# Performance work log

Measured on AMD Instinct MI355X. Metric: run time of the kernel, lower is better.

## Reference

```python
import jax, jax.numpy as jnp
import numpy as np

N_NODES = 50000
N_EDGES = 800000
IN, HID, OUT = 128, [128, 128], 64


def setup_inputs() -> dict:
    key = jax.random.key(0)
    ks = jax.random.split(key, 10)
    inp = {
        'in_feat': jax.random.normal(ks[0], (N_NODES, IN), dtype=jnp.float32),
        'src': jax.random.randint(ks[1], (N_EDGES,), 0, N_NODES, dtype=jnp.int32),
        'dst': jax.random.randint(ks[2], (N_EDGES,), 0, N_NODES, dtype=jnp.int32),
    }
    dims = [IN] + HID + [OUT]  # [128,128,128,64]
    for i in range(3):
        fan_in = dims[i]
        inp[f'W{i}'] = jax.random.normal(ks[3 + i], (dims[i + 1], dims[i]), dtype=jnp.float32) / np.sqrt(fan_in)
        inp[f'b{i}'] = jnp.zeros((dims[i + 1],), dtype=jnp.float32)
    return inp


def _sage_gcn_layer(x, W, b, src, dst, n_nodes):
    # DGL SAGEConv aggregator_type='gcn':
    #   neigh = segment_sum of src feats over dst edges (graph already has self-loops)
    #   h = (neigh + x) / (in_degree + 1); out = h @ W.T + b
    msg = x[src]                                             # [E, d] gather
    neigh = jax.ops.segment_sum(msg, dst, num_segments=n_nodes)
    deg = jax.ops.segment_sum(jnp.ones(src.shape[0], x.dtype), dst, num_segments=n_nodes)
    h = (neigh + x) / (deg[:, None] + 1.0)
    return h @ W.T + b


def reference(in_feat, src, dst, W0, b0, W1, b1, W2, b2):
    n = in_feat.shape[0]
    # remove_self_loop + add_self_loop -> exactly one self loop per node
    loop = jnp.arange(n, dtype=src.dtype)
    src_f = jnp.concatenate([src, loop])
    dst_f = jnp.concatenate([dst, loop])
    # Dropout(0.5) is identity in eval mode.
    h = in_feat
    h = jax.nn.relu(_sage_gcn_layer(h, W0, b0, src_f, dst_f, n))
    h = jax.nn.relu(_sage_gcn_layer(h, W1, b1, src_f, dst_f, n))
    h = _sage_gcn_layer(h, W2, b2, src_f, dst_f, n)
    return h
```

## Files before the change

kernel.cpp:

```cpp
#include <hip/hip_runtime.h>
#include <hip/hip_bf16.h>


#define NFEAT 128
#define BKT_CAP 12288
#define CHUNK 64

using bf16x8 = __attribute__((ext_vector_type(8))) short;
using f32x4  = __attribute__((ext_vector_type(4))) float;

__device__ __forceinline__ ushort f2bf(float f) {
    unsigned u = __float_as_uint(f);
    u = (u + 0x7fffu + ((u >> 16) & 1u)) >> 16;
    return (ushort)u;
}
__device__ __forceinline__ float bflo(unsigned v) { return __uint_as_float(v << 16); }
__device__ __forceinline__ float bfhi(unsigned v) { return __uint_as_float(v & 0xffff0000u); }

__device__ __forceinline__ int xcc_id() {
    int x;
    asm volatile("s_getreg_b32 %0, hwreg(HW_REG_XCC_ID)" : "=s"(x));
    return x & 7;
}


__global__ __launch_bounds__(1024) void k_zero_words(int* __restrict__ p, int n) {
    int i = threadIdx.x;
    if (i < n) p[i] = 0;
}

__global__ __launch_bounds__(256) void k_bin(const int* __restrict__ src, const int* __restrict__ dst,
                                             int* __restrict__ gcur, unsigned* __restrict__ pairs, int ne) {
    __shared__ int lcnt[128];
    __shared__ int lbase[128];
    int tid = threadIdx.x;
    if (tid < 128) lcnt[tid] = 0;
    __syncthreads();
    int e0 = blockIdx.x * 4096;
    int myrank[16];
    int mybkt[16];
    unsigned mypair[16];
    #pragma unroll
    for (int i = 0; i < 16; ++i) {
        int e = e0 + tid + i * 256;
        if (e < ne) {
            int s = src[e], d = dst[e];
            int b = d >> 9;
            mybkt[i]  = b;
            mypair[i] = (unsigned)(s & 0xffff) | ((unsigned)(d & 511) << 16);
            myrank[i] = atomicAdd(&lcnt[b], 1);
        } else mybkt[i] = -1;
    }
    __syncthreads();
    if (tid < 128) lbase[tid] = lcnt[tid] ? atomicAdd(&gcur[tid], lcnt[tid]) : 0;
    __syncthreads();
    #pragma unroll
    for (int i = 0; i < 16; ++i) {
        if (mybkt[i] >= 0) {
            int pos = lbase[mybkt[i]] + myrank[i];
            if (pos < BKT_CAP) pairs[(size_t)mybkt[i] * BKT_CAP + pos] = mypair[i];
        }
    }
}

__global__ __launch_bounds__(256) void k_cnt(const unsigned* __restrict__ pairs, const int* __restrict__ gcur,
                                             int* __restrict__ cnt, int n) {
    __shared__ int lcnt[512];
    int b = blockIdx.x, tid = threadIdx.x;
    for (int i = tid; i < 512; i += 256) lcnt[i] = 0;
    __syncthreads();
    int m = gcur[b];
    if (m > BKT_CAP) m = BKT_CAP;
    const unsigned* p = pairs + (size_t)b * BKT_CAP;
    for (int i = tid; i < m; i += 256) atomicAdd(&lcnt[p[i] >> 16], 1);
    __syncthreads();
    int base = b * 512;
    for (int i = tid; i < 512; i += 256) {
        int node = base + i;
        if (node < n) cnt[node] = lcnt[i];
    }
}

__global__ __launch_bounds__(1024) void k_scan_part(const int* __restrict__ cnt, int* __restrict__ part,
                                                    int* __restrict__ tots, int n) {
    __shared__ int wtot[16];
    __shared__ int wpre[16];
    int tid  = threadIdx.x;
    int lane = tid & 63;
    int wv   = tid >> 6;
    int i    = blockIdx.x * 1024 + tid;
    int v    = (i < n) ? cnt[i] : 0;
    int val  = v;
    #pragma unroll
    for (int off = 1; off < 64; off <<= 1) {
        int t = __shfl_up(val, off);
        if (lane >= off) val += t;
    }
    if (lane == 63) wtot[wv] = val;
    __syncthreads();
    if (tid == 0) {
        int s = 0;
        #pragma unroll
        for (int w = 0; w < 16; ++w) { wpre[w] = s; s += wtot[w]; }
        tots[blockIdx.x] = s;
    }
    __syncthreads();
    int excl = val - v + wpre[wv];
    if (i < n) part[i] = excl;
}

__global__ __launch_bounds__(1024) void k_scan_tops(int* __restrict__ tots, int* __restrict__ total_out, int nch) {
    __shared__ int wtot[16];
    __shared__ int wpre[16];
    int tid  = threadIdx.x;
    int lane = tid & 63;
    int wv   = tid >> 6;
    int v    = (tid < nch) ? tots[tid] : 0;
    int val  = v;
    #pragma unroll
    for (int off = 1; off < 64; off <<= 1) {
        int t = __shfl_up(val, off);
        if (lane >= off) val += t;
    }
    if (lane == 63) wtot[wv] = val;
    __syncthreads();
    if (tid == 0) {
        int s = 0;
        #pragma unroll
        for (int w = 0; w < 16; ++w) { wpre[w] = s; s += wtot[w]; }
        *total_out = s;
    }
    __syncthreads();
    int excl = val - v + wpre[wv];
    if (tid < nch) tots[tid] = excl;
}

__global__ __launch_bounds__(1024) void k_scan_add(int* __restrict__ offs, const int* __restrict__ tots, int n) {
    int i = blockIdx.x * 1024 + threadIdx.x;
    if (i < n) offs[i] += tots[blockIdx.x];
}

__global__ __launch_bounds__(256) void k_scatter(const unsigned* __restrict__ pairs, const int* __restrict__ gcur,
                                                 const int* __restrict__ offs, ushort* __restrict__ esrc, int n) {
    __shared__ int lcur[512];
    __shared__ int loffs[512];
    int b = blockIdx.x, tid = threadIdx.x;
    int base = b * 512;
    for (int i = tid; i < 512; i += 256) {
        lcur[i] = 0;
        int node = base + i;
        loffs[i] = (node < n) ? offs[node] : 0;
    }
    __syncthreads();
    int m = gcur[b];
    if (m > BKT_CAP) m = BKT_CAP;
    const unsigned* p = pairs + (size_t)b * BKT_CAP;
    for (int i = tid; i < m; i += 256) {
        unsigned pr = p[i];
        int dlow = pr >> 16;
        int r = atomicAdd(&lcur[dlow], 1);
        esrc[loffs[dlow] + r] = (ushort)(pr & 0xffffu);
    }
}


__global__ __launch_bounds__(1024) void k_dsort_win(const int* __restrict__ cnt, int* __restrict__ perm, int n) {
    __shared__ int hist[256];
    __shared__ int hcur[256];
    __shared__ int wtot[16];
    __shared__ int wpre[16];
    int tid  = threadIdx.x;
    int base = blockIdx.x * 1024;
    if (tid < 256) hist[tid] = 0;
    __syncthreads();
    int i = base + tid;
    bool act = i < n;
    int d = 0, rank = 0;
    if (act) {
        d = cnt[i];
        if (d > 255) d = 255;
        rank = atomicAdd(&hist[d], 1);
    }
    __syncthreads();
    int lane = tid & 63;
    int wv   = tid >> 6;
    int v    = (tid < 256) ? hist[tid] : 0;
    int val  = v;
    #pragma unroll
    for (int off = 1; off < 64; off <<= 1) {
        int t = __shfl_up(val, off);
        if (lane >= off) val += t;
    }
    if (lane == 63) wtot[wv] = val;
    __syncthreads();
    if (tid == 0) {
        int s = 0;
        #pragma unroll
        for (int w = 0; w < 4; ++w) { wpre[w] = s; s += wtot[w]; }
    }
    __syncthreads();
    if (tid < 256) hcur[tid] = val - v + wpre[wv];
    __syncthreads();
    if (act) perm[base + hcur[d] + rank] = i;
}


__global__ __launch_bounds__(256) void k_cast3(const float* __restrict__ a, int na,
                                               const float* __restrict__ b, int nb,
                                               const float* __restrict__ c, int nc,
                                               ushort* __restrict__ out) {
    int i = blockIdx.x * 256 + threadIdx.x;
    if (i >= na + nb + nc) return;
    float v = (i < na) ? a[i] : ((i < na + nb) ? b[i - na] : c[i - na - nb]);
    out[i] = f2bf(v);
}


template <typename InT, int N, bool PLANES_IN>
__global__ __launch_bounds__(256) void k_gemm_mfma(const InT* __restrict__ X, const ushort* __restrict__ Wb,
                                                   ushort* __restrict__ Y, int M) {
    int w    = threadIdx.x >> 6;
    int lane = threadIdx.x & 63;
    int rowf = blockIdx.x * 64 + w * 16 + (lane & 15);
    int kb   = (lane >> 4) * 8;

    bf16x8 a[4];
    if (rowf < M) {
        #pragma unroll
        for (int ks = 0; ks < 4; ++ks) {
            if constexpr (PLANES_IN) {
                a[ks] = *(const bf16x8*)((const ushort*)X + (size_t)ks * M * 32 + (size_t)rowf * 32 + kb);
            } else {
                const float* xp = (const float*)X + (size_t)rowf * 128 + ks * 32 + kb;
                float4 f0 = *(const float4*)xp;
                float4 f1 = *(const float4*)(xp + 4);
                bf16x8 t;
                t[0] = f2bf(f0.x); t[1] = f2bf(f0.y); t[2] = f2bf(f0.z); t[3] = f2bf(f0.w);
                t[4] = f2bf(f1.x); t[5] = f2bf(f1.y); t[6] = f2bf(f1.z); t[7] = f2bf(f1.w);
                a[ks] = t;
            }
        }
    } else {
        #pragma unroll
        for (int ks = 0; ks < 4; ++ks) {
            bf16x8 z = {0, 0, 0, 0, 0, 0, 0, 0};
            a[ks] = z;
        }
    }

    constexpr int NT = N / 16;
    f32x4 acc[NT];
    #pragma unroll
    for (int nt = 0; nt < NT; ++nt) acc[nt] = (f32x4){0.f, 0.f, 0.f, 0.f};

    #pragma unroll
    for (int nt = 0; nt < NT; ++nt) {
        const ushort* wp = Wb + (size_t)(nt * 16 + (lane & 15)) * 128 + kb;
        #pragma unroll
        for (int ks = 0; ks < 4; ++ks) {
            bf16x8 b = *(const bf16x8*)(wp + ks * 32);
            acc[nt] = __builtin_amdgcn_mfma_f32_16x16x32_bf16(a[ks], b, acc[nt], 0, 0, 0);
        }
    }

    int c  = lane & 15;
    int r0 = blockIdx.x * 64 + w * 16 + (lane >> 4) * 4;
    #pragma unroll
    for (int j = 0; j < 4; ++j) {
        int r = r0 + j;
        if (r < M) {
            #pragma unroll
            for (int nt = 0; nt < NT; ++nt)
                Y[(size_t)(nt >> 1) * M * 32 + (size_t)r * 32 + (nt & 1) * 16 + c] = (ushort)f2bf(acc[nt][j]);
        }
    }
}


#define ACC8(T)  { a0 += bflo((T).x); a1 += bfhi((T).x); a2 += bflo((T).y); a3 += bfhi((T).y); \
                   a4 += bflo((T).z); a5 += bfhi((T).z); a6 += bflo((T).w); a7 += bfhi((T).w); }

template <bool RELU>
__global__ __launch_bounds__(256) void k_agg128(const ushort* __restrict__ Yp, const int* __restrict__ offs,
                                                const ushort* __restrict__ esrc, const float* __restrict__ bias,
                                                ushort* __restrict__ Zp, const int* __restrict__ perm,
                                                int* __restrict__ qh, int n, int nchunk) {
    __shared__ int sQ, sT;
    if (threadIdx.x == 0) {
        int pref = xcc_id() & 3;
        int t = -1, qsel = 0;
        #pragma unroll
        for (int a = 0; a < 4; ++a) {
            int cand = (pref + a) & 3;
            int tt = atomicAdd(&qh[cand * 16], 1);
            if (tt < nchunk) { qsel = cand; t = tt; break; }
        }
        sQ = qsel; sT = t;
    }
    __syncthreads();
    int q = sQ, t = sT;
    if (t < 0) return;
    int lane = threadIdx.x & 63;
    int wv   = threadIdx.x >> 6;
    int g    = lane >> 2;
    int sub  = lane & 3;
    int idx  = t * CHUNK + wv * 16 + g;
    bool active = idx < n;
    int nd = 0, start = 0, rem = 0;
    if (active) {
        nd    = perm[idx];
        start = offs[nd];
        rem   = offs[nd + 1] - start;
    }
    const uint4* Y4 = (const uint4*)(Yp + (size_t)q * n * 32);
    uint4*       Z4 = (uint4*)(Zp + (size_t)q * n * 32);

    float a0 = 0.f, a1 = 0.f, a2 = 0.f, a3 = 0.f, a4 = 0.f, a5 = 0.f, a6 = 0.f, a7 = 0.f;

    int minrem = rem, maxrem = rem;
    #pragma unroll
    for (int m = 4; m < 64; m <<= 1) {
        minrem = min(minrem, __shfl_xor(minrem, m));
        maxrem = max(maxrem, __shfl_xor(maxrem, m));
    }

    int r = 0;
    for (; r + 8 <= minrem; r += 8) {
        int e = start + r;
        int s0 = esrc[e],     s1 = esrc[e + 1], s2 = esrc[e + 2], s3 = esrc[e + 3];
        int s4 = esrc[e + 4], s5 = esrc[e + 5], s6 = esrc[e + 6], s7 = esrc[e + 7];
        uint4 t0 = Y4[(size_t)s0 * 4 + sub];
        uint4 t1 = Y4[(size_t)s1 * 4 + sub];
        uint4 t2 = Y4[(size_t)s2 * 4 + sub];
        uint4 t3 = Y4[(size_t)s3 * 4 + sub];
        uint4 t4 = Y4[(size_t)s4 * 4 + sub];
        uint4 t5 = Y4[(size_t)s5 * 4 + sub];
        uint4 t6 = Y4[(size_t)s6 * 4 + sub];
        uint4 t7 = Y4[(size_t)s7 * 4 + sub];
        ACC8(t0); ACC8(t1); ACC8(t2); ACC8(t3); ACC8(t4); ACC8(t5); ACC8(t6); ACC8(t7);
    }
    for (; r + 4 <= minrem; r += 4) {
        int e = start + r;
        int s0 = esrc[e], s1 = esrc[e + 1], s2 = esrc[e + 2], s3 = esrc[e + 3];
        uint4 t0 = Y4[(size_t)s0 * 4 + sub];
        uint4 t1 = Y4[(size_t)s1 * 4 + sub];
        uint4 t2 = Y4[(size_t)s2 * 4 + sub];
        uint4 t3 = Y4[(size_t)s3 * 4 + sub];
        ACC8(t0); ACC8(t1); ACC8(t2); ACC8(t3);
    }
    for (; r < maxrem; r += 4) {
        #pragma unroll
        for (int c = 0; c < 4; ++c) {
            int rr = r + c;
            bool val = rr < rem;
            int e = val ? (start + rr) : 0;
            int s = esrc[e];
            uint4 tv = Y4[(size_t)s * 4 + sub];
            if (!val) { tv.x = 0u; tv.y = 0u; tv.z = 0u; tv.w = 0u; }
            ACC8(tv);
        }
    }

    if (active) {
        float scale = 1.0f / (float)(rem + 2);
        uint4 sf = Y4[(size_t)nd * 4 + sub];
        int f0 = q * 32 + sub * 8;
        float4 bA = *(const float4*)&bias[f0];
        float4 bB = *(const float4*)&bias[f0 + 4];
        float r0 = (a0 + 2.f * bflo(sf.x)) * scale + bA.x;
        float r1 = (a1 + 2.f * bfhi(sf.x)) * scale + bA.y;
        float r2 = (a2 + 2.f * bflo(sf.y)) * scale + bA.z;
        float r3 = (a3 + 2.f * bfhi(sf.y)) * scale + bA.w;
        float r4 = (a4 + 2.f * bflo(sf.z)) * scale + bB.x;
        float r5 = (a5 + 2.f * bfhi(sf.z)) * scale + bB.y;
        float r6 = (a6 + 2.f * bflo(sf.w)) * scale + bB.z;
        float r7 = (a7 + 2.f * bfhi(sf.w)) * scale + bB.w;
        if (RELU) {
            r0 = fmaxf(r0, 0.f); r1 = fmaxf(r1, 0.f); r2 = fmaxf(r2, 0.f); r3 = fmaxf(r3, 0.f);
            r4 = fmaxf(r4, 0.f); r5 = fmaxf(r5, 0.f); r6 = fmaxf(r6, 0.f); r7 = fmaxf(r7, 0.f);
        }
        uint4 o;
        o.x = (unsigned)f2bf(r0) | ((unsigned)f2bf(r1) << 16);
        o.y = (unsigned)f2bf(r2) | ((unsigned)f2bf(r3) << 16);
        o.z = (unsigned)f2bf(r4) | ((unsigned)f2bf(r5) << 16);
        o.w = (unsigned)f2bf(r6) | ((unsigned)f2bf(r7) << 16);
        Z4[(size_t)nd * 4 + sub] = o;
    }
}

__global__ __launch_bounds__(256) void k_agg64(const ushort* __restrict__ Yp, const int* __restrict__ offs,
                                               const ushort* __restrict__ esrc, const float* __restrict__ bias,
                                               float* __restrict__ Z, const int* __restrict__ perm,
                                               int* __restrict__ qh, int n, int nchunk) {
    __shared__ int sQ, sT;
    if (threadIdx.x == 0) {
        int pref = xcc_id() & 1;
        int t = -1, qsel = 0;
        #pragma unroll
        for (int a = 0; a < 2; ++a) {
            int cand = (pref + a) & 1;
            int tt = atomicAdd(&qh[cand * 16], 1);
            if (tt < nchunk) { qsel = cand; t = tt; break; }
        }
        sQ = qsel; sT = t;
    }
    __syncthreads();
    int h = sQ, t = sT;
    if (t < 0) return;
    int lane = threadIdx.x & 63;
    int wv   = threadIdx.x >> 6;
    int g    = lane >> 2;
    int sub  = lane & 3;
    int idx  = t * CHUNK + wv * 16 + g;
    bool active = idx < n;
    int nd = 0, start = 0, rem = 0;
    if (active) {
        nd    = perm[idx];
        start = offs[nd];
        rem   = offs[nd + 1] - start;
    }
    const uint4* Y4 = (const uint4*)(Yp + (size_t)h * n * 32);

    float a0 = 0.f, a1 = 0.f, a2 = 0.f, a3 = 0.f, a4 = 0.f, a5 = 0.f, a6 = 0.f, a7 = 0.f;

    int minrem = rem, maxrem = rem;
    #pragma unroll
    for (int m = 4; m < 64; m <<= 1) {
        minrem = min(minrem, __shfl_xor(minrem, m));
        maxrem = max(maxrem, __shfl_xor(maxrem, m));
    }

    int r = 0;
    for (; r + 8 <= minrem; r += 8) {
        int e = start + r;
        int s0 = esrc[e],     s1 = esrc[e + 1], s2 = esrc[e + 2], s3 = esrc[e + 3];
        int s4 = esrc[e + 4], s5 = esrc[e + 5], s6 = esrc[e + 6], s7 = esrc[e + 7];
        uint4 t0 = Y4[(size_t)s0 * 4 + sub];
        uint4 t1 = Y4[(size_t)s1 * 4 + sub];
        uint4 t2 = Y4[(size_t)s2 * 4 + sub];
        uint4 t3 = Y4[(size_t)s3 * 4 + sub];
        uint4 t4 = Y4[(size_t)s4 * 4 + sub];
        uint4 t5 = Y4[(size_t)s5 * 4 + sub];
        uint4 t6 = Y4[(size_t)s6 * 4 + sub];
        uint4 t7 = Y4[(size_t)s7 * 4 + sub];
        ACC8(t0); ACC8(t1); ACC8(t2); ACC8(t3); ACC8(t4); ACC8(t5); ACC8(t6); ACC8(t7);
    }
    for (; r + 4 <= minrem; r += 4) {
        int e = start + r;
        int s0 = esrc[e], s1 = esrc[e + 1], s2 = esrc[e + 2], s3 = esrc[e + 3];
        uint4 t0 = Y4[(size_t)s0 * 4 + sub];
        uint4 t1 = Y4[(size_t)s1 * 4 + sub];
        uint4 t2 = Y4[(size_t)s2 * 4 + sub];
        uint4 t3 = Y4[(size_t)s3 * 4 + sub];
        ACC8(t0); ACC8(t1); ACC8(t2); ACC8(t3);
    }
    for (; r < maxrem; r += 4) {
        #pragma unroll
        for (int c = 0; c < 4; ++c) {
            int rr = r + c;
            bool val = rr < rem;
            int e = val ? (start + rr) : 0;
            int s = esrc[e];
            uint4 tv = Y4[(size_t)s * 4 + sub];
            if (!val) { tv.x = 0u; tv.y = 0u; tv.z = 0u; tv.w = 0u; }
            ACC8(tv);
        }
    }

    if (active) {
        float scale = 1.0f / (float)(rem + 2);
        uint4 sf = Y4[(size_t)nd * 4 + sub];
        int f0 = h * 32 + sub * 8;
        float4 bA = *(const float4*)&bias[f0];
        float4 bB = *(const float4*)&bias[f0 + 4];
        float4 oA, oB;
        oA.x = (a0 + 2.f * bflo(sf.x)) * scale + bA.x;
        oA.y = (a1 + 2.f * bfhi(sf.x)) * scale + bA.y;
        oA.z = (a2 + 2.f * bflo(sf.y)) * scale + bA.z;
        oA.w = (a3 + 2.f * bfhi(sf.y)) * scale + bA.w;
        oB.x = (a4 + 2.f * bflo(sf.z)) * scale + bB.x;
        oB.y = (a5 + 2.f * bfhi(sf.z)) * scale + bB.y;
        oB.z = (a6 + 2.f * bflo(sf.w)) * scale + bB.z;
        oB.w = (a7 + 2.f * bfhi(sf.w)) * scale + bB.w;
        float* zr = Z + (size_t)nd * 64 + f0;
        *(float4*)zr       = oA;
        *(float4*)(zr + 4) = oB;
    }
}


extern "C" void kernel_launch(void* const* d_in, const int* in_sizes, int n_in,
                              void* d_out, int out_size, void* d_ws, size_t ws_size,
                              hipStream_t stream) {
    const float* in_feat = (const float*)d_in[0];
    const int*   src     = (const int*)d_in[1];
    const int*   dst     = (const int*)d_in[2];
    const float* W0      = (const float*)d_in[3];
    const float* b0      = (const float*)d_in[4];
    const float* W1      = (const float*)d_in[5];
    const float* b1      = (const float*)d_in[6];
    const float* W2      = (const float*)d_in[7];
    const float* b2      = (const float*)d_in[8];
    float* out = (float*)d_out;

    const int n  = in_sizes[0] / NFEAT;
    const int ne = in_sizes[1];
    const int nch = (n + 1023) / 1024;
    const int NB  = (n + 511) >> 9;
    const int nchunk = (n + CHUNK - 1) / CHUNK;

    int* offs       = (int*)d_ws;
    int* tots       = offs + (((n + 1) + 3) & ~3);
    int* gcur       = tots + 1024;
    int* qh         = gcur + 128;
    int* cnt        = qh + 192;
    int* perm       = cnt + ((n + 3) & ~3);
    unsigned* pairs = (unsigned*)(perm + ((n + 3) & ~3));
    ushort* esrc    = (ushort*)(pairs + (size_t)128 * BKT_CAP);
    ushort* Wb      = esrc + ((ne + 15) & ~15);
    ushort* Ybuf    = Wb + 40960;
    ushort* Zbuf    = Ybuf + (size_t)n * NFEAT;

    k_zero_words<<<1, 1024, 0, stream>>>(gcur, 128 + 192);
    k_bin<<<(ne + 4095) / 4096, 256, 0, stream>>>(src, dst, gcur, pairs, ne);
    k_cnt<<<NB, 256, 0, stream>>>(pairs, gcur, cnt, n);
    k_dsort_win<<<nch, 1024, 0, stream>>>(cnt, perm, n);
    k_scan_part<<<nch, 1024, 0, stream>>>(cnt, offs, tots, n);
    k_scan_tops<<<1, 1024, 0, stream>>>(tots, offs + n, nch);
    k_scan_add<<<nch, 1024, 0, stream>>>(offs, tots, n);
    k_scatter<<<NB, 256, 0, stream>>>(pairs, gcur, offs, esrc, n);

    k_cast3<<<(40960 + 255) / 256, 256, 0, stream>>>(W0, 16384, W1, 16384, W2, 8192, Wb);
    const ushort* Wb0 = Wb;
    const ushort* Wb1 = Wb + 16384;
    const ushort* Wb2 = Wb + 32768;

    const int gg = (n + 63) / 64;

    k_gemm_mfma<float, 128, false><<<gg, 256, 0, stream>>>(in_feat, Wb0, Ybuf, n);
    k_agg128<true><<<4 * nchunk, 256, 0, stream>>>(Ybuf, offs, esrc, b0, Zbuf, perm, qh, n, nchunk);
    k_gemm_mfma<ushort, 128, true><<<gg, 256, 0, stream>>>(Zbuf, Wb1, Ybuf, n);
    k_agg128<true><<<4 * nchunk, 256, 0, stream>>>(Ybuf, offs, esrc, b1, Zbuf, perm, qh + 64, n, nchunk);
    k_gemm_mfma<ushort, 64, true><<<gg, 256, 0, stream>>>(Zbuf, Wb2, Ybuf, n);
    k_agg64<<<2 * nchunk, 256, 0, stream>>>(Ybuf, offs, esrc, b2, out, perm, qh + 128, n, nchunk);

    (void)ws_size; (void)n_in; (void)out_size;
}
```

Baseline: 222.1 us.

## Pad CSR rows to multiples of eight with sentinel zero row for branchless gathers

```diff
diff --git a/kernel.cpp b/kernel.cpp
--- a/kernel.cpp
+++ b/kernel.cpp
@@ -24,10 +24,20 @@
 }
 
 
-__global__ __launch_bounds__(1024) void k_zero_words(int* __restrict__ p, int n) {
-    int i = threadIdx.x;
-    if (i < n) p[i] = 0;
-}
+__global__ __launch_bounds__(256) void k_init(unsigned* __restrict__ esrc_u32, int fillN, unsigned sent2,
+                                              int* __restrict__ ctl, ushort* __restrict__ Ybuf, int n) {
+    int i = blockIdx.x * 256 + threadIdx.x;
+    if (i < fillN) {
+        esrc_u32[i] = sent2;
+    } else if (i < fillN + 320) {
+        ctl[i - fillN] = 0;
+    } else if (i < fillN + 320 + 64) {
+        int j = i - fillN - 320;
+        int p = j >> 4, k = j & 15;
+        ((unsigned*)(Ybuf + (size_t)p * (n + 1) * 32 + (size_t)n * 32))[k] = 0u;
+    }
+}
+
 
 __global__ __launch_bounds__(256) void k_bin(const int* __restrict__ src, const int* __restrict__ dst,
                                              int* __restrict__ gcur, unsigned* __restrict__ pairs, int ne) {
@@ -81,32 +91,67 @@
     }
 }
 
-__global__ __launch_bounds__(1024) void k_scan_part(const int* __restrict__ cnt, int* __restrict__ part,
-                                                    int* __restrict__ tots, int n) {
+__global__ __launch_bounds__(1024) void k_prep_win(const int* __restrict__ cnt, int* __restrict__ perm,
+                                                   int* __restrict__ part, int* __restrict__ tots, int n) {
+    __shared__ int hist[256];
+    __shared__ int hcur[256];
     __shared__ int wtot[16];
     __shared__ int wpre[16];
     int tid  = threadIdx.x;
     int lane = tid & 63;
     int wv   = tid >> 6;
-    int i    = blockIdx.x * 1024 + tid;
-    int v    = (i < n) ? cnt[i] : 0;
-    int val  = v;
-    #pragma unroll
-    for (int off = 1; off < 64; off <<= 1) {
-        int t = __shfl_up(val, off);
-        if (lane >= off) val += t;
-    }
-    if (lane == 63) wtot[wv] = val;
-    __syncthreads();
-    if (tid == 0) {
-        int s = 0;
-        #pragma unroll
-        for (int w = 0; w < 16; ++w) { wpre[w] = s; s += wtot[w]; }
-        tots[blockIdx.x] = s;
-    }
-    __syncthreads();
-    int excl = val - v + wpre[wv];
-    if (i < n) part[i] = excl;
+    int base = blockIdx.x * 1024;
+    if (tid < 256) hist[tid] = 0;
+    __syncthreads();
+    int i = base + tid;
+    bool act = i < n;
+    int c = 0, d = 0, rank = 0;
+    if (act) {
+        c = cnt[i];
+        d = c > 255 ? 255 : c;
+        rank = atomicAdd(&hist[d], 1);
+    }
+    __syncthreads();
+    {
+        int v = (tid < 256) ? hist[tid] : 0;
+        int val = v;
+        #pragma unroll
+        for (int off = 1; off < 64; off <<= 1) {
+            int t = __shfl_up(val, off);
+            if (lane >= off) val += t;
+        }
+        if (lane == 63) wtot[wv] = val;
+        __syncthreads();
+        if (tid == 0) {
+            int s = 0;
+            #pragma unroll
+            for (int w = 0; w < 4; ++w) { wpre[w] = s; s += wtot[w]; }
+        }
+        __syncthreads();
+        if (tid < 256) hcur[tid] = val - v + wpre[wv];
+        __syncthreads();
+        if (act) perm[base + hcur[d] + rank] = i;
+        __syncthreads();
+    }
+    {
+        int p = act ? ((c + 7) & ~7) : 0;
+        int val = p;
+        #pragma unroll
+        for (int off = 1; off < 64; off <<= 1) {
+            int t = __shfl_up(val, off);
+            if (lane >= off) val += t;
+        }
+        if (lane == 63) wtot[wv] = val;
+        __syncthreads();
+        if (tid == 0) {
+            int s = 0;
+            #pragma unroll
+            for (int w = 0; w < 16; ++w) { wpre[w] = s; s += wtot[w]; }
+            tots[blockIdx.x] = s;
+        }
+        __syncthreads();
+        if (act) part[i] = val - p + wpre[wv];
+    }
 }
 
 __global__ __launch_bounds__(1024) void k_scan_tops(int* __restrict__ tots, int* __restrict__ total_out, int nch) {
@@ -164,47 +209,6 @@
 }
 
 
-__global__ __launch_bounds__(1024) void k_dsort_win(const int* __restrict__ cnt, int* __restrict__ perm, int n) {
-    __shared__ int hist[256];
-    __shared__ int hcur[256];
-    __shared__ int wtot[16];
-    __shared__ int wpre[16];
-    int tid  = threadIdx.x;
-    int base = blockIdx.x * 1024;
-    if (tid < 256) hist[tid] = 0;
-    __syncthreads();
-    int i = base + tid;
-    bool act = i < n;
-    int d = 0, rank = 0;
-    if (act) {
-        d = cnt[i];
-        if (d > 255) d = 255;
-        rank = atomicAdd(&hist[d], 1);
-    }
-    __syncthreads();
-    int lane = tid & 63;
-    int wv   = tid >> 6;
-    int v    = (tid < 256) ? hist[tid] : 0;
-    int val  = v;
-    #pragma unroll
-    for (int off = 1; off < 64; off <<= 1) {
-        int t = __shfl_up(val, off);
-        if (lane >= off) val += t;
-    }
-    if (lane == 63) wtot[wv] = val;
-    __syncthreads();
-    if (tid == 0) {
-        int s = 0;
-        #pragma unroll
-        for (int w = 0; w < 4; ++w) { wpre[w] = s; s += wtot[w]; }
-    }
-    __syncthreads();
-    if (tid < 256) hcur[tid] = val - v + wpre[wv];
-    __syncthreads();
-    if (act) perm[base + hcur[d] + rank] = i;
-}
-
-
 __global__ __launch_bounds__(256) void k_cast3(const float* __restrict__ a, int na,
                                                const float* __restrict__ b, int nb,
                                                const float* __restrict__ c, int nc,
@@ -218,7 +222,7 @@
 
 template <typename InT, int N, bool PLANES_IN>
 __global__ __launch_bounds__(256) void k_gemm_mfma(const InT* __restrict__ X, const ushort* __restrict__ Wb,
-                                                   ushort* __restrict__ Y, int M) {
+                                                   ushort* __restrict__ Y, int M, int Mp) {
     int w    = threadIdx.x >> 6;
     int lane = threadIdx.x & 63;
     int rowf = blockIdx.x * 64 + w * 16 + (lane & 15);
@@ -229,7 +233,7 @@
         #pragma unroll
         for (int ks = 0; ks < 4; ++ks) {
             if constexpr (PLANES_IN) {
-                a[ks] = *(const bf16x8*)((const ushort*)X + (size_t)ks * M * 32 + (size_t)rowf * 32 + kb);
+                a[ks] = *(const bf16x8*)((const ushort*)X + (size_t)ks * Mp * 32 + (size_t)rowf * 32 + kb);
             } else {
                 const float* xp = (const float*)X + (size_t)rowf * 128 + ks * 32 + kb;
                 float4 f0 = *(const float4*)xp;
@@ -271,7 +275,7 @@
         if (r < M) {
             #pragma unroll
             for (int nt = 0; nt < NT; ++nt)
-                Y[(size_t)(nt >> 1) * M * 32 + (size_t)r * 32 + (nt & 1) * 16 + c] = (ushort)f2bf(acc[nt][j]);
+                Y[(size_t)(nt >> 1) * Mp * 32 + (size_t)r * 32 + (nt & 1) * 16 + c] = (ushort)f2bf(acc[nt][j]);
         }
     }
 }
@@ -282,9 +286,10 @@
 
 template <bool RELU>
 __global__ __launch_bounds__(256) void k_agg128(const ushort* __restrict__ Yp, const int* __restrict__ offs,
-                                                const ushort* __restrict__ esrc, const float* __restrict__ bias,
-                                                ushort* __restrict__ Zp, const int* __restrict__ perm,
-                                                int* __restrict__ qh, int n, int nchunk) {
+                                                const int* __restrict__ cnt, const ushort* __restrict__ esrc,
+                                                const float* __restrict__ bias, ushort* __restrict__ Zp,
+                                                const int* __restrict__ perm, int* __restrict__ qh,
+                                                int n, int nchunk) {
     __shared__ int sQ, sT;
     if (threadIdx.x == 0) {
         int pref = xcc_id() & 3;
@@ -306,29 +311,27 @@
     int sub  = lane & 3;
     int idx  = t * CHUNK + wv * 16 + g;
     bool active = idx < n;
-    int nd = 0, start = 0, rem = 0;
+    int nd = 0, start = 0, deg = 0;
     if (active) {
         nd    = perm[idx];
         start = offs[nd];
-        rem   = offs[nd + 1] - start;
-    }
-    const uint4* Y4 = (const uint4*)(Yp + (size_t)q * n * 32);
-    uint4*       Z4 = (uint4*)(Zp + (size_t)q * n * 32);
+        deg   = cnt[nd];
+    }
+    const uint4* Y4 = (const uint4*)(Yp + (size_t)q * (n + 1) * 32);
+    uint4*       Z4 = (uint4*)(Zp + (size_t)q * (n + 1) * 32);
 
     float a0 = 0.f, a1 = 0.f, a2 = 0.f, a3 = 0.f, a4 = 0.f, a5 = 0.f, a6 = 0.f, a7 = 0.f;
 
-    int minrem = rem, maxrem = rem;
-    #pragma unroll
-    for (int m = 4; m < 64; m <<= 1) {
-        minrem = min(minrem, __shfl_xor(minrem, m));
-        maxrem = max(maxrem, __shfl_xor(maxrem, m));
-    }
-
-    int r = 0;
-    for (; r + 8 <= minrem; r += 8) {
-        int e = start + r;
-        int s0 = esrc[e],     s1 = esrc[e + 1], s2 = esrc[e + 2], s3 = esrc[e + 3];
-        int s4 = esrc[e + 4], s5 = esrc[e + 5], s6 = esrc[e + 6], s7 = esrc[e + 7];
+    int nblk = active ? ((deg + 7) >> 3) : 0;
+    const uint4* ep = (const uint4*)(esrc + start);
+    uint4 ib = ep[0];
+    #pragma unroll 2
+    for (int b = 0; b < nblk; ++b) {
+        uint4 ibn = ep[b + 1];
+        unsigned s0 = ib.x & 0xffffu, s1 = ib.x >> 16;
+        unsigned s2 = ib.y & 0xffffu, s3 = ib.y >> 16;
+        unsigned s4 = ib.z & 0xffffu, s5 = ib.z >> 16;
+        unsigned s6 = ib.w & 0xffffu, s7 = ib.w >> 16;
         uint4 t0 = Y4[(size_t)s0 * 4 + sub];
         uint4 t1 = Y4[(size_t)s1 * 4 + sub];
         uint4 t2 = Y4[(size_t)s2 * 4 + sub];
@@ -338,31 +341,11 @@
         uint4 t6 = Y4[(size_t)s6 * 4 + sub];
         uint4 t7 = Y4[(size_t)s7 * 4 + sub];
         ACC8(t0); ACC8(t1); ACC8(t2); ACC8(t3); ACC8(t4); ACC8(t5); ACC8(t6); ACC8(t7);
-    }
-    for (; r + 4 <= minrem; r += 4) {
-        int e = start + r;
-        int s0 = esrc[e], s1 = esrc[e + 1], s2 = esrc[e + 2], s3 = esrc[e + 3];
-        uint4 t0 = Y4[(size_t)s0 * 4 + sub];
-        uint4 t1 = Y4[(size_t)s1 * 4 + sub];
-        uint4 t2 = Y4[(size_t)s2 * 4 + sub];
-        uint4 t3 = Y4[(size_t)s3 * 4 + sub];
-        ACC8(t0); ACC8(t1); ACC8(t2); ACC8(t3);
-    }
-    for (; r < maxrem; r += 4) {
-        #pragma unroll
-        for (int c = 0; c < 4; ++c) {
-            int rr = r + c;
-            bool val = rr < rem;
-            int e = val ? (start + rr) : 0;
-            int s = esrc[e];
-            uint4 tv = Y4[(size_t)s * 4 + sub];
-            if (!val) { tv.x = 0u; tv.y = 0u; tv.z = 0u; tv.w = 0u; }
-            ACC8(tv);
-        }
+        ib = ibn;
     }
 
     if (active) {
-        float scale = 1.0f / (float)(rem + 2);
+        float scale = 1.0f / (float)(deg + 2);
         uint4 sf = Y4[(size_t)nd * 4 + sub];
         int f0 = q * 32 + sub * 8;
         float4 bA = *(const float4*)&bias[f0];
@@ -389,9 +372,10 @@
 }
 
 __global__ __launch_bounds__(256) void k_agg64(const ushort* __restrict__ Yp, const int* __restrict__ offs,
-                                               const ushort* __restrict__ esrc, const float* __restrict__ bias,
-                                               float* __restrict__ Z, const int* __restrict__ perm,
-                                               int* __restrict__ qh, int n, int nchunk) {
+                                               const int* __restrict__ cnt, const ushort* __restrict__ esrc,
+                                               const float* __restrict__ bias, float* __restrict__ Z,
+                                               const int* __restrict__ perm, int* __restrict__ qh,
+                                               int n, int nchunk) {
     __shared__ int sQ, sT;
     if (threadIdx.x == 0) {
         int pref = xcc_id() & 1;
@@ -413,28 +397,26 @@
     int sub  = lane & 3;
     int idx  = t * CHUNK + wv * 16 + g;
     bool active = idx < n;
-    int nd = 0, start = 0, rem = 0;
+    int nd = 0, start = 0, deg = 0;
     if (active) {
         nd    = perm[idx];
         start = offs[nd];
-        rem   = offs[nd + 1] - start;
-    }
-    const uint4* Y4 = (const uint4*)(Yp + (size_t)h * n * 32);
+        deg   = cnt[nd];
+    }
+    const uint4* Y4 = (const uint4*)(Yp + (size_t)h * (n + 1) * 32);
 
     float a0 = 0.f, a1 = 0.f, a2 = 0.f, a3 = 0.f, a4 = 0.f, a5 = 0.f, a6 = 0.f, a7 = 0.f;
 
-    int minrem = rem, maxrem = rem;
-    #pragma unroll
-    for (int m = 4; m < 64; m <<= 1) {
-        minrem = min(minrem, __shfl_xor(minrem, m));
-        maxrem = max(maxrem, __shfl_xor(maxrem, m));
-    }
-
-    int r = 0;
-    for (; r + 8 <= minrem; r += 8) {
-        int e = start + r;
-        int s0 = esrc[e],     s1 = esrc[e + 1], s2 = esrc[e + 2], s3 = esrc[e + 3];
-        int s4 = esrc[e + 4], s5 = esrc[e + 5], s6 = esrc[e + 6], s7 = esrc[e + 7];
+    int nblk = active ? ((deg + 7) >> 3) : 0;
+    const uint4* ep = (const uint4*)(esrc + start);
+    uint4 ib = ep[0];
+    #pragma unroll 2
+    for (int b = 0; b < nblk; ++b) {
+        uint4 ibn = ep[b + 1];
+        unsigned s0 = ib.x & 0xffffu, s1 = ib.x >> 16;
+        unsigned s2 = ib.y & 0xffffu, s3 = ib.y >> 16;
+        unsigned s4 = ib.z & 0xffffu, s5 = ib.z >> 16;
+        unsigned s6 = ib.w & 0xffffu, s7 = ib.w >> 16;
         uint4 t0 = Y4[(size_t)s0 * 4 + sub];
         uint4 t1 = Y4[(size_t)s1 * 4 + sub];
         uint4 t2 = Y4[(size_t)s2 * 4 + sub];
@@ -444,31 +426,11 @@
         uint4 t6 = Y4[(size_t)s6 * 4 + sub];
         uint4 t7 = Y4[(size_t)s7 * 4 + sub];
         ACC8(t0); ACC8(t1); ACC8(t2); ACC8(t3); ACC8(t4); ACC8(t5); ACC8(t6); ACC8(t7);
-    }
-    for (; r + 4 <= minrem; r += 4) {
-        int e = start + r;
-        int s0 = esrc[e], s1 = esrc[e + 1], s2 = esrc[e + 2], s3 = esrc[e + 3];
-        uint4 t0 = Y4[(size_t)s0 * 4 + sub];
-        uint4 t1 = Y4[(size_t)s1 * 4 + sub];
-        uint4 t2 = Y4[(size_t)s2 * 4 + sub];
-        uint4 t3 = Y4[(size_t)s3 * 4 + sub];
-        ACC8(t0); ACC8(t1); ACC8(t2); ACC8(t3);
-    }
-    for (; r < maxrem; r += 4) {
-        #pragma unroll
-        for (int c = 0; c < 4; ++c) {
-            int rr = r + c;
-            bool val = rr < rem;
-            int e = val ? (start + rr) : 0;
-            int s = esrc[e];
-            uint4 tv = Y4[(size_t)s * 4 + sub];
-            if (!val) { tv.x = 0u; tv.y = 0u; tv.z = 0u; tv.w = 0u; }
-            ACC8(tv);
-        }
+        ib = ibn;
     }
 
     if (active) {
-        float scale = 1.0f / (float)(rem + 2);
+        float scale = 1.0f / (float)(deg + 2);
         uint4 sf = Y4[(size_t)nd * 4 + sub];
         int f0 = h * 32 + sub * 8;
         float4 bA = *(const float4*)&bias[f0];
@@ -508,6 +470,7 @@
     const int nch = (n + 1023) / 1024;
     const int NB  = (n + 511) >> 9;
     const int nchunk = (n + CHUNK - 1) / CHUNK;
+    const int escap = (ne + 8 * n + 31) & ~15;
 
     int* offs       = (int*)d_ws;
     int* tots       = offs + (((n + 1) + 3) & ~3);
@@ -517,15 +480,17 @@
     int* perm       = cnt + ((n + 3) & ~3);
     unsigned* pairs = (unsigned*)(perm + ((n + 3) & ~3));
     ushort* esrc    = (ushort*)(pairs + (size_t)128 * BKT_CAP);
-    ushort* Wb      = esrc + ((ne + 15) & ~15);
+    ushort* Wb      = esrc + escap;
     ushort* Ybuf    = Wb + 40960;
-    ushort* Zbuf    = Ybuf + (size_t)n * NFEAT;
-
-    k_zero_words<<<1, 1024, 0, stream>>>(gcur, 128 + 192);
+    ushort* Zbuf    = Ybuf + (size_t)(n + 1) * NFEAT;
+
+    const int fillN = escap / 2;
+    const unsigned sent2 = ((unsigned)n << 16) | (unsigned)n;
+    k_init<<<(fillN + 320 + 64 + 255) / 256, 256, 0, stream>>>((unsigned*)esrc, fillN, sent2, gcur, Ybuf, n);
+
     k_bin<<<(ne + 4095) / 4096, 256, 0, stream>>>(src, dst, gcur, pairs, ne);
     k_cnt<<<NB, 256, 0, stream>>>(pairs, gcur, cnt, n);
-    k_dsort_win<<<nch, 1024, 0, stream>>>(cnt, perm, n);
-    k_scan_part<<<nch, 1024, 0, stream>>>(cnt, offs, tots, n);
+    k_prep_win<<<nch, 1024, 0, stream>>>(cnt, perm, offs, tots, n);
     k_scan_tops<<<1, 1024, 0, stream>>>(tots, offs + n, nch);
     k_scan_add<<<nch, 1024, 0, stream>>>(offs, tots, n);
     k_scatter<<<NB, 256, 0, stream>>>(pairs, gcur, offs, esrc, n);
@@ -536,13 +501,14 @@
     const ushort* Wb2 = Wb + 32768;
 
     const int gg = (n + 63) / 64;
-
-    k_gemm_mfma<float, 128, false><<<gg, 256, 0, stream>>>(in_feat, Wb0, Ybuf, n);
-    k_agg128<true><<<4 * nchunk, 256, 0, stream>>>(Ybuf, offs, esrc, b0, Zbuf, perm, qh, n, nchunk);
-    k_gemm_mfma<ushort, 128, true><<<gg, 256, 0, stream>>>(Zbuf, Wb1, Ybuf, n);
-    k_agg128<true><<<4 * nchunk, 256, 0, stream>>>(Ybuf, offs, esrc, b1, Zbuf, perm, qh + 64, n, nchunk);
-    k_gemm_mfma<ushort, 64, true><<<gg, 256, 0, stream>>>(Zbuf, Wb2, Ybuf, n);
-    k_agg64<<<2 * nchunk, 256, 0, stream>>>(Ybuf, offs, esrc, b2, out, perm, qh + 128, n, nchunk);
+    const int Mp = n + 1;
+
+    k_gemm_mfma<float, 128, false><<<gg, 256, 0, stream>>>(in_feat, Wb0, Ybuf, n, Mp);
+    k_agg128<true><<<4 * nchunk, 256, 0, stream>>>(Ybuf, offs, cnt, esrc, b0, Zbuf, perm, qh, n, nchunk);
+    k_gemm_mfma<ushort, 128, true><<<gg, 256, 0, stream>>>(Zbuf, Wb1, Ybuf, n, Mp);
+    k_agg128<true><<<4 * nchunk, 256, 0, stream>>>(Ybuf, offs, cnt, esrc, b1, Zbuf, perm, qh + 64, n, nchunk);
+    k_gemm_mfma<ushort, 64, true><<<gg, 256, 0, stream>>>(Zbuf, Wb2, Ybuf, n, Mp);
+    k_agg64<<<2 * nchunk, 256, 0, stream>>>(Ybuf, offs, cnt, esrc, b2, out, perm, qh + 128, n, nchunk);
 
     (void)ws_size; (void)n_in; (void)out_size;
 }
```

New measurement: 221.2 us. About the same (-0.4%).
